# Kernel tuning notes

Measured on AMD Instinct MI355X. Metric: run time of the kernel, lower is better.

Reference implementation:

```python
import jax, jax.numpy as jnp
import numpy as np

B, S, HID, NH = 2, 2048, 2048, 16
HD = HID // NH          # head_size = 128
ROPE_THETA = 10000.0
SCALING = HD ** -0.5


def setup_inputs() -> dict:
    key = jax.random.key(0)
    ks = jax.random.split(key, 8)
    std = 1.0 / np.sqrt(HID)
    inp = {
        "hidden_states": jax.random.normal(ks[0], (B, S, HID), jnp.float32),
        "positions": jnp.broadcast_to(jnp.arange(S, dtype=jnp.int32), (B, S)),
        "wq": jax.random.normal(ks[1], (HID, HID), jnp.float32) * std,
        "bq": jax.random.normal(ks[2], (HID,), jnp.float32) * 0.02,
        "wk": jax.random.normal(ks[3], (HID, HID), jnp.float32) * std,
        "bk": jax.random.normal(ks[4], (HID,), jnp.float32) * 0.02,
        "wv": jax.random.normal(ks[5], (HID, HID), jnp.float32) * std,
        "bv": jax.random.normal(ks[6], (HID,), jnp.float32) * 0.02,
        "wc": jax.random.normal(ks[7], (HID, HID), jnp.float32) * std,
    }
    return inp


def _rope_neox(x, positions):
    # x: [B, S, NH, HD]; positions: [B, S] int
    half = HD // 2
    inv_freq = 1.0 / (ROPE_THETA ** (jnp.arange(half, dtype=jnp.float32) * (2.0 / HD)))
    freqs = positions.astype(jnp.float32)[..., None] * inv_freq      # [B,S,half]
    cos = jnp.cos(freqs)[:, :, None, :]                               # [B,S,1,half]
    sin = jnp.sin(freqs)[:, :, None, :]
    x1, x2 = x[..., :half], x[..., half:]
    return jnp.concatenate([x1 * cos - x2 * sin, x2 * cos + x1 * sin], axis=-1)


def reference(hidden_states, positions, wq, bq, wk, bk, wv, bv, wc):
    # fused QKV projections
    q = hidden_states @ wq + bq
    k = hidden_states @ wk + bk
    v = hidden_states @ wv + bv
    q = q.reshape(B, S, NH, HD)
    k = k.reshape(B, S, NH, HD)
    v = v.reshape(B, S, NH, HD)
    # neox-style rotary embedding over full head dim
    q = _rope_neox(q, positions)
    k = _rope_neox(k, positions)
    # causal self-attention (prefill path of RadixAttention)
    scores = jnp.einsum("bqhd,bkhd->bhqk", q, k) * SCALING
    causal = jnp.tril(jnp.ones((S, S), dtype=bool))
    scores = jnp.where(causal, scores, jnp.finfo(scores.dtype).min)
    probs = jax.nn.softmax(scores, axis=-1)
    attn = jnp.einsum("bhqk,bkhd->bqhd", probs, v).reshape(B, S, HID)
    # output projection (no bias)
    return attn @ wc
```

## Files before the change

kernel.cpp:

```cpp
#include <hip/hip_runtime.h>
#include <stdint.h>

constexpr int Bsz = 2;
constexpr int Ssz = 2048;
constexpr int Hid = 2048;
constexpr int NHd = 16;
constexpr int Hd  = 128;
constexpr int Mrows = Bsz * Ssz;

typedef __bf16 bf16;
typedef __bf16 bf16x8 __attribute__((ext_vector_type(8)));
typedef __bf16 bf16x4 __attribute__((ext_vector_type(4)));
typedef float  f32x4  __attribute__((ext_vector_type(4)));
typedef float  f32x16 __attribute__((ext_vector_type(16)));

__device__ __forceinline__ void gload_lds16(const bf16* g, bf16* l) {
  __builtin_amdgcn_global_load_lds((const __attribute__((address_space(1))) void*)g,
                                   (__attribute__((address_space(3))) void*)l, 16, 0, 0);
}

__device__ __forceinline__ uint32_t pkbf(bf16 a, bf16 b) {
  union { bf16 hh[2]; uint32_t u; } x;
  x.hh[0] = a; x.hh[1] = b;
  return x.u;
}
__device__ __forceinline__ uint32_t pkff(float a, float b) {
  return pkbf((bf16)a, (bf16)b);
}

__global__ void k_cvt(const float* __restrict__ in, bf16* __restrict__ out, int n4) {
  int i = blockIdx.x * blockDim.x + threadIdx.x;
  if (i >= n4) return;
  float4 v = ((const float4*)in)[i];
  bf16x4 o = { (bf16)v.x, (bf16)v.y, (bf16)v.z, (bf16)v.w };
  ((bf16x4*)out)[i] = o;
}

__global__ void k_wtrans(const float* __restrict__ w0, const float* __restrict__ w1,
                         const float* __restrict__ w2, const float* __restrict__ w3,
                         bf16* __restrict__ out) {
  __shared__ float tile[32][33];
  int z = blockIdx.z;
  const float* w = (z == 0) ? w0 : (z == 1) ? w1 : (z == 2) ? w2 : w3;
  bf16* o = out + (size_t)z * Hid * Hid;
  int n0 = blockIdx.x * 32, k0 = blockIdx.y * 32;
  int tx = threadIdx.x, ty = threadIdx.y;
#pragma unroll
  for (int i = 0; i < 4; i++)
    tile[ty + i * 8][tx] = w[(size_t)(k0 + ty + i * 8) * Hid + n0 + tx];
  __syncthreads();
#pragma unroll
  for (int i = 0; i < 4; i++)
    o[(size_t)(n0 + ty + i * 8) * Hid + k0 + tx] = (bf16)tile[tx][ty + i * 8];
}

__device__ __forceinline__ bf16x8 rdfrag(const bf16* t, int row, int kslot) {
  return *(const bf16x8*)((const char*)t + row * 128 + (((kslot ^ (row & 7)) & 7) << 4));
}

template <int NB>
__device__ __forceinline__ void stageN(const bf16* g, bf16* l, int w, int lane) {
  const int rsub = lane >> 3;
  const int slot = (lane & 7) ^ rsub;
#pragma unroll
  for (int j = 0; j < NB; ++j) {
    const int blk = w * NB + j;
    gload_lds16(g + (size_t)(blk * 8 + rsub) * Hid + slot * 8, l + blk * 512);
  }
}

#define PH_SYNC()                                      \
  __builtin_amdgcn_s_barrier();                        \
  asm volatile("s_waitcnt lgkmcnt(0)" ::: "memory");   \
  __builtin_amdgcn_sched_barrier(0);

template <int MODE, int CHM, int CHN>
__global__ __launch_bounds__(512, 1) void k_gemm(const bf16* __restrict__ A,
                                                 const bf16* __restrict__ Bt,
                                                 const float* __restrict__ biasq,
                                                 const float* __restrict__ biask,
                                                 const float* __restrict__ biasv,
                                                 bf16* __restrict__ Qo, bf16* __restrict__ Ko,
                                                 bf16* __restrict__ Vo, float* __restrict__ Fo) {
  constexpr int KK = Hid;
  constexpr int NT = KK / 64;
  __shared__ bf16 smA[3][256 * 64];
  __shared__ bf16 smB[3][128 * 64];
  const int hw = blockIdx.y * gridDim.x + blockIdx.x;
  const int chunk = hw & 7, within = hw >> 3;
  const int chunk_rows = gridDim.y / CHM;
  const int cr = chunk % chunk_rows, cc = chunk / chunk_rows;
  const int mt = cr * CHM + within % CHM;
  const int nt = cc * CHN + within / CHM;
  const int m0 = mt * 256, n0 = nt * 128;
  const int tid = threadIdx.x, lane = tid & 63, w = tid >> 6;
  const int wm = w >> 1, wn = w & 1;
  const int frow = lane & 15, a4 = lane >> 4;
  const bf16* Ag = A + (size_t)m0 * KK;
  const bf16* Bg = Bt + (size_t)n0 * KK;
  f32x4 acc[4][4] = {};
  stageN<4>(Ag, smA[0], w, lane);
  stageN<2>(Bg, smB[0], w, lane);
  stageN<4>(Ag + 64, smA[1], w, lane);
  stageN<2>(Bg + 64, smB[1], w, lane);
  asm volatile("s_waitcnt vmcnt(6)" ::: "memory");
  __builtin_amdgcn_s_barrier();
  for (int kt = 0; kt < NT; ++kt) {
    const bf16* At  = smA[kt % 3];
    const bf16* Btl = smB[kt % 3];
    bf16* As2 = smA[(kt + 2) % 3];
    bf16* Bs2 = smB[(kt + 2) % 3];
    const int kn2 = (kt + 2 < NT ? kt + 2 : kt) * 64;
    bf16x8 af[2][2], bfr[4][2];
#pragma unroll
    for (int mi = 0; mi < 2; ++mi)
#pragma unroll
      for (int kk = 0; kk < 2; ++kk)
        af[mi][kk] = rdfrag(At, wm * 64 + mi * 16 + frow, kk * 4 + a4);
#pragma unroll
    for (int ni = 0; ni < 4; ++ni)
#pragma unroll
      for (int kk = 0; kk < 2; ++kk)
        bfr[ni][kk] = rdfrag(Btl, wn * 64 + ni * 16 + frow, kk * 4 + a4);
    stageN<4>(Ag + kn2, As2, w, lane);
    PH_SYNC();
    __builtin_amdgcn_s_setprio(1);
#pragma unroll
    for (int mi = 0; mi < 2; ++mi)
#pragma unroll
      for (int ni = 0; ni < 4; ++ni)
#pragma unroll
        for (int kk = 0; kk < 2; ++kk)
          acc[mi][ni] = __builtin_amdgcn_mfma_f32_16x16x32_bf16(
              af[mi][kk], bfr[ni][kk], acc[mi][ni], 0, 0, 0);
    __builtin_amdgcn_s_setprio(0);
    __builtin_amdgcn_s_barrier();
#pragma unroll
    for (int mi = 0; mi < 2; ++mi)
#pragma unroll
      for (int kk = 0; kk < 2; ++kk)
        af[mi][kk] = rdfrag(At, wm * 64 + (2 + mi) * 16 + frow, kk * 4 + a4);
    stageN<2>(Bg + kn2, Bs2, w, lane);
    PH_SYNC();
    __builtin_amdgcn_s_setprio(1);
#pragma unroll
    for (int mi = 0; mi < 2; ++mi)
#pragma unroll
      for (int ni = 0; ni < 4; ++ni)
#pragma unroll
        for (int kk = 0; kk < 2; ++kk)
          acc[2 + mi][ni] = __builtin_amdgcn_mfma_f32_16x16x32_bf16(
              af[mi][kk], bfr[ni][kk], acc[2 + mi][ni], 0, 0, 0);
    __builtin_amdgcn_s_setprio(0);
    asm volatile("s_waitcnt vmcnt(6)" ::: "memory");
    __builtin_amdgcn_sched_barrier(0);
    __builtin_amdgcn_s_barrier();
  }
  if (MODE == 0) {
    const int z = n0 >> 11;
    const float* bias = (z == 0) ? biasq : (z == 1) ? biask : biasv;
    bf16* o = (z == 0) ? Qo : (z == 1) ? Ko : Vo;
    const float oscale = (z == 1) ? (float)(0.08838834764831845 * 1.4426950408889634) : 1.0f;
#pragma unroll
    for (int ni = 0; ni < 4; ++ni) {
      const int col = n0 + wn * 64 + ni * 16 + frow;
      const float bb_ = bias[col & 2047];
      const int h = (col >> 7) & 15, hd = col & (Hd - 1);
#pragma unroll
      for (int mi = 0; mi < 4; ++mi) {
#pragma unroll
        for (int r = 0; r < 4; ++r) {
          const int row = m0 + wm * 64 + mi * 16 + a4 * 4 + r;
          const int bb = row >> 11, ss = row & (Ssz - 1);
          o[(((size_t)bb * NHd + h) * Ssz + ss) * Hd + hd] = (bf16)((acc[mi][ni][r] + bb_) * oscale);
        }
      }
    }
  } else {
#pragma unroll
    for (int mi = 0; mi < 4; ++mi)
#pragma unroll
      for (int ni = 0; ni < 4; ++ni) {
        const int col = n0 + wn * 64 + ni * 16 + frow;
#pragma unroll
        for (int r = 0; r < 4; ++r) {
          const int row = m0 + wm * 64 + mi * 16 + a4 * 4 + r;
          Fo[(size_t)row * Hid + col] = acc[mi][ni][r];
        }
      }
  }
}

__global__ void k_rope(bf16* __restrict__ Q, bf16* __restrict__ Kk, const int* __restrict__ pos) {
  const int idx = blockIdx.x * 256 + threadIdx.x;
  const int i = idx & 63;
  const int s = (idx >> 6) & (Ssz - 1);
  const int bh = idx >> 17;
  const int b = bh >> 4;
  const float p = (float)pos[b * Ssz + s];
  const float f = p * exp2f(-(float)i * 0.20762050593046014f);
  float sn, cs;
  sincosf(f, &sn, &cs);
  const size_t base = ((size_t)bh * Ssz + s) * Hd;
  float x1 = (float)Q[base + i], x2 = (float)Q[base + i + 64];
  Q[base + i]      = (bf16)(x1 * cs - x2 * sn);
  Q[base + i + 64] = (bf16)(x2 * cs + x1 * sn);
  x1 = (float)Kk[base + i]; x2 = (float)Kk[base + i + 64];
  Kk[base + i]      = (bf16)(x1 * cs - x2 * sn);
  Kk[base + i + 64] = (bf16)(x2 * cs + x1 * sn);
}

__global__ __launch_bounds__(256, 2) void k_attn(const bf16* __restrict__ Qg,
                                                 const bf16* __restrict__ Kg,
                                                 const bf16* __restrict__ Vg,
                                                 bf16* __restrict__ AO) {
  const int bh = blockIdx.y;
  int qc = blockIdx.x;
  if (bh & 1) qc = 15 - qc;
  const int tid = threadIdx.x, lane = tid & 63, w = tid >> 6;
  const int l31 = lane & 31, h = lane >> 5;
  __shared__ bf16 Ks[2][64 * 128];
  __shared__ bf16 Vt[2][128 * 72];
  const size_t hbase = (size_t)bh * Ssz * Hd;
  const int q0 = qc * 128 + w * 32;
  bf16x8 qf[8];
  {
    const bf16* qp = Qg + hbase + (size_t)(q0 + l31) * Hd + h * 8;
#pragma unroll
    for (int c = 0; c < 8; c++) qf[c] = *(const bf16x8*)(qp + c * 16);
  }
  float m = -1e30f, lsum = 0.f;
  f32x16 o[4] = {};
  const int NT = 2 * (qc + 1);
  const int r4  = (tid >> 4) << 2;
  const int hd0 = (tid & 15) << 3;
  bf16x8 vv[4];
#pragma unroll
  for (int p = 0; p < 4; p++)
    vv[p] = *(const bf16x8*)(Vg + hbase + (size_t)(r4 + p) * Hd + hd0);
  __builtin_amdgcn_sched_barrier(0);
#pragma unroll
  for (int i = 0; i < 4; i++) {
    const int db  = (w * 4 + i) * 1024 + (lane << 4);
    const int row = db >> 8;
    const int cb  = (db & 255) ^ ((row & 7) << 4);
    gload_lds16(Kg + hbase + row * Hd + (cb >> 1), Ks[0] + (w * 4 + i) * 512);
  }
  for (int t = 0; t < NT; ++t) {
    const int kv0 = t * 64;
    const int cur = t & 1;
    asm volatile("s_waitcnt vmcnt(4)" ::: "memory");
#pragma unroll
    for (int j = 0; j < 8; j++) {
      uint2 wv;
      wv.x = pkbf(vv[0][j], vv[1][j]);
      wv.y = pkbf(vv[2][j], vv[3][j]);
      const int hd = hd0 + j;
      const int cb = (r4 * 2) ^ (((hd >> 3) & 7) << 4);
      *(uint2*)((char*)(Vt[cur]) + hd * 144 + cb) = wv;
    }
    const int tn = (t + 1 < NT) ? t + 1 : t;
    const size_t nb = (size_t)tn * 64;
#pragma unroll
    for (int p = 0; p < 4; p++)
      vv[p] = *(const bf16x8*)(Vg + hbase + (nb + r4 + p) * Hd + hd0);
    __builtin_amdgcn_sched_barrier(0);
#pragma unroll
    for (int i = 0; i < 4; i++) {
      const int db  = (w * 4 + i) * 1024 + (lane << 4);
      const int row = db >> 8;
      const int cb  = (db & 255) ^ ((row & 7) << 4);
      gload_lds16(Kg + hbase + (nb + row) * Hd + (cb >> 1), Ks[cur ^ 1] + (w * 4 + i) * 512);
    }
    asm volatile("s_waitcnt vmcnt(8) lgkmcnt(0)" ::: "memory");
    __builtin_amdgcn_sched_barrier(0);
    __builtin_amdgcn_s_barrier();
    if (kv0 <= q0 + 31) {
      const bf16* KsC = Ks[cur];
      const bf16* VtC = Vt[cur];
      f32x16 s0 = {}, s1 = {};
#pragma unroll
      for (int c = 0; c < 8; c++) {
        const int cb = (c * 32 + h * 16) ^ ((l31 & 7) << 4);
        bf16x8 k0 = *(const bf16x8*)((const char*)KsC + l31 * 256 + cb);
        bf16x8 k1 = *(const bf16x8*)((const char*)KsC + (32 + l31) * 256 + cb);
        s0 = __builtin_amdgcn_mfma_f32_32x32x16_bf16(k0, qf[c], s0, 0, 0, 0);
        s1 = __builtin_amdgcn_mfma_f32_32x32x16_bf16(k1, qf[c], s1, 0, 0, 0);
      }
      if (kv0 + 63 > q0) {
        const int qg = q0 + l31;
        const int kb = kv0 + 4 * h;
#pragma unroll
        for (int r = 0; r < 16; r++) {
          const int cr = (r & 3) + 8 * (r >> 2);
          if (kb + cr > qg)      s0[r] = -1e30f;
          if (kb + 32 + cr > qg) s1[r] = -1e30f;
        }
      }
      float tm = s0[0];
#pragma unroll
      for (int r = 1; r < 16; r++) tm = fmaxf(tm, s0[r]);
#pragma unroll
      for (int r = 0; r < 16; r++) tm = fmaxf(tm, s1[r]);
      tm = fmaxf(tm, __shfl_xor(tm, 32));
      if (!__all(tm - m <= 8.0f)) {
        const float mn = fmaxf(m, tm);
        const float rs = exp2f(m - mn);
        m = mn; lsum *= rs;
#pragma unroll
        for (int ct = 0; ct < 4; ct++)
#pragma unroll
          for (int r = 0; r < 16; r++) o[ct][r] *= rs;
      }
      float ps = 0.f;
#pragma unroll
      for (int r = 0; r < 16; r++) { s0[r] = exp2f(s0[r] - m); ps += s0[r]; }
#pragma unroll
      for (int r = 0; r < 16; r++) { s1[r] = exp2f(s1[r] - m); ps += s1[r]; }
      ps += __shfl_xor(ps, 32);
      lsum += ps;
      uint32_t gw[8][2];
#pragma unroll
      for (int g = 0; g < 4; g++) {
        gw[g][0]     = pkff(s0[4 * g], s0[4 * g + 1]);
        gw[g][1]     = pkff(s0[4 * g + 2], s0[4 * g + 3]);
        gw[4 + g][0] = pkff(s1[4 * g], s1[4 * g + 1]);
        gw[4 + g][1] = pkff(s1[4 * g + 2], s1[4 * g + 3]);
      }
#pragma unroll
      for (int kc = 0; kc < 4; kc++) {
        const uint32_t a0 = gw[2 * kc][0], a1 = gw[2 * kc][1];
        const uint32_t b0 = gw[2 * kc + 1][0], b1 = gw[2 * kc + 1][1];
        const uint32_t sd0 = h ? a0 : b0, sd1 = h ? a1 : b1;
        const uint32_t r0 = (uint32_t)__shfl_xor((int)sd0, 32);
        const uint32_t r1 = (uint32_t)__shfl_xor((int)sd1, 32);
        union { uint32_t u[4]; bf16x8 v; } pa;
        pa.u[0] = h ? r0 : a0; pa.u[1] = h ? r1 : a1;
        pa.u[2] = h ? b0 : r0; pa.u[3] = h ? b1 : r1;
#pragma unroll
        for (int ct = 0; ct < 4; ct++) {
          const int row = ct * 32 + l31;
          const int cb = (kc * 32 + h * 16) ^ (((row >> 3) & 7) << 4);
          bf16x8 vf = *(const bf16x8*)((const char*)VtC + row * 144 + cb);
          o[ct] = __builtin_amdgcn_mfma_f32_32x32x16_bf16(pa.v, vf, o[ct], 0, 0, 0);
        }
      }
    }
    __builtin_amdgcn_s_barrier();
  }
  const float linv = 1.0f / lsum;
  float li[16];
#pragma unroll
  for (int r = 0; r < 16; r++)
    li[r] = __shfl(linv, (r & 3) + 8 * (r >> 2) + 4 * h);
  const int b = bh >> 4, hh = bh & 15;
#pragma unroll
  for (int ct = 0; ct < 4; ct++) {
#pragma unroll
    for (int r = 0; r < 16; r++) {
      const int qrow = q0 + (r & 3) + 8 * (r >> 2) + 4 * h;
      AO[((size_t)b * Ssz + qrow) * Hid + hh * Hd + ct * 32 + l31] = (bf16)(o[ct][r] * li[r]);
    }
  }
}

extern "C" void kernel_launch(void* const* d_in, const int* in_sizes, int n_in,
                              void* d_out, int out_size, void* d_ws, size_t ws_size,
                              hipStream_t stream) {
  (void)in_sizes; (void)n_in; (void)out_size; (void)ws_size;
  const float* hidden   = (const float*)d_in[0];
  const int*   positions= (const int*)d_in[1];
  const float* wq = (const float*)d_in[2];
  const float* bq = (const float*)d_in[3];
  const float* wk = (const float*)d_in[4];
  const float* bk = (const float*)d_in[5];
  const float* wv = (const float*)d_in[6];
  const float* bv = (const float*)d_in[7];
  const float* wc = (const float*)d_in[8];
  float* out = (float*)d_out;

  char* ws = (char*)d_ws;
  bf16* WT  = (bf16*)ws;
  bf16* Hbf = (bf16*)(ws + (size_t)4 * Hid * Hid * 2);
  bf16* Qb  = (bf16*)(ws + (size_t)4 * Hid * Hid * 2 + (size_t)Mrows * Hid * 2);
  bf16* Kb  = Qb + (size_t)Mrows * Hid;
  bf16* Vb  = Kb + (size_t)Mrows * Hid;

  k_cvt<<<dim3(Mrows * Hid / 4 / 256), dim3(256), 0, stream>>>(hidden, Hbf, Mrows * Hid / 4);
  k_wtrans<<<dim3(Hid / 32, Hid / 32, 4), dim3(32, 8), 0, stream>>>(wq, wk, wv, wc, WT);
  k_gemm<0, 8, 12><<<dim3(48, 16), dim3(512), 0, stream>>>(
      Hbf, WT, bq, bk, bv, Qb, Kb, Vb, nullptr);
  k_rope<<<dim3(Bsz * NHd * Ssz * 64 / 256), dim3(256), 0, stream>>>(Qb, Kb, positions);
  k_attn<<<dim3(16, Bsz * NHd), dim3(256), 0, stream>>>(Qb, Kb, Vb, Hbf );
  k_gemm<1, 4, 8><<<dim3(16, 16), dim3(512), 0, stream>>>(
      Hbf, WT + (size_t)3 * Hid * Hid, nullptr, nullptr, nullptr,
      nullptr, nullptr, nullptr, out);
}
```

Before: 293.5 us.

## Enlarge GEMM tiles to 256x256 with double-buffered LDS and four-phase loop

Both GEMM launches now use 256x256 output tiles in place of 256x128. The LDS buffering drops from triple to double buffering, and each K step is split into four MFMA phases that overlap the next A and B loads. The goal is more data reuse per LDS byte and fewer reloads from global memory. In exchange each wave holds twice the accumulators, the waitcnt before each barrier is now a full vmcnt(0) that exposes load latency, and the grids shrink to 384 and 128 blocks, which may leave CUs idle on a 256-CU part.

```diff
diff --git a/kernel.cpp b/kernel.cpp
--- a/kernel.cpp
+++ b/kernel.cpp
@@ -75,7 +75,7 @@
   __builtin_amdgcn_sched_barrier(0);
 
 template <int MODE, int CHM, int CHN>
-__global__ __launch_bounds__(512, 1) void k_gemm(const bf16* __restrict__ A,
+__global__ __launch_bounds__(512, 2) void k_gemm(const bf16* __restrict__ A,
                                                  const bf16* __restrict__ Bt,
                                                  const float* __restrict__ biasq,
                                                  const float* __restrict__ biask,
@@ -84,77 +84,64 @@
                                                  bf16* __restrict__ Vo, float* __restrict__ Fo) {
   constexpr int KK = Hid;
   constexpr int NT = KK / 64;
-  __shared__ bf16 smA[3][256 * 64];
-  __shared__ bf16 smB[3][128 * 64];
+  __shared__ bf16 smA[2][256 * 64];
+  __shared__ bf16 smB[2][256 * 64];
   const int hw = blockIdx.y * gridDim.x + blockIdx.x;
   const int chunk = hw & 7, within = hw >> 3;
   const int chunk_rows = gridDim.y / CHM;
   const int cr = chunk % chunk_rows, cc = chunk / chunk_rows;
   const int mt = cr * CHM + within % CHM;
   const int nt = cc * CHN + within / CHM;
-  const int m0 = mt * 256, n0 = nt * 128;
+  const int m0 = mt * 256, n0 = nt * 256;
   const int tid = threadIdx.x, lane = tid & 63, w = tid >> 6;
-  const int wm = w >> 1, wn = w & 1;
+  const int wm = w >> 2, wn = w & 3;
   const int frow = lane & 15, a4 = lane >> 4;
   const bf16* Ag = A + (size_t)m0 * KK;
   const bf16* Bg = Bt + (size_t)n0 * KK;
-  f32x4 acc[4][4] = {};
+  f32x4 acc[8][4] = {};
   stageN<4>(Ag, smA[0], w, lane);
-  stageN<2>(Bg, smB[0], w, lane);
-  stageN<4>(Ag + 64, smA[1], w, lane);
-  stageN<2>(Bg + 64, smB[1], w, lane);
-  asm volatile("s_waitcnt vmcnt(6)" ::: "memory");
+  stageN<4>(Bg, smB[0], w, lane);
+  asm volatile("s_waitcnt vmcnt(0)" ::: "memory");
   __builtin_amdgcn_s_barrier();
   for (int kt = 0; kt < NT; ++kt) {
-    const bf16* At  = smA[kt % 3];
-    const bf16* Btl = smB[kt % 3];
-    bf16* As2 = smA[(kt + 2) % 3];
-    bf16* Bs2 = smB[(kt + 2) % 3];
-    const int kn2 = (kt + 2 < NT ? kt + 2 : kt) * 64;
-    bf16x8 af[2][2], bfr[4][2];
-#pragma unroll
-    for (int mi = 0; mi < 2; ++mi)
+    const bf16* At  = smA[kt & 1];
+    const bf16* Btl = smB[kt & 1];
+    bf16* As2 = smA[(kt + 1) & 1];
+    bf16* Bs2 = smB[(kt + 1) & 1];
+    const int kn = (kt + 1 < NT ? kt + 1 : kt) * 64;
+    bf16x8 bfr[4][2];
+#pragma unroll
+    for (int nf = 0; nf < 4; ++nf)
 #pragma unroll
       for (int kk = 0; kk < 2; ++kk)
-        af[mi][kk] = rdfrag(At, wm * 64 + mi * 16 + frow, kk * 4 + a4);
-#pragma unroll
-    for (int ni = 0; ni < 4; ++ni)
-#pragma unroll
-      for (int kk = 0; kk < 2; ++kk)
-        bfr[ni][kk] = rdfrag(Btl, wn * 64 + ni * 16 + frow, kk * 4 + a4);
-    stageN<4>(Ag + kn2, As2, w, lane);
-    PH_SYNC();
-    __builtin_amdgcn_s_setprio(1);
-#pragma unroll
-    for (int mi = 0; mi < 2; ++mi)
-#pragma unroll
-      for (int ni = 0; ni < 4; ++ni)
+        bfr[nf][kk] = rdfrag(Btl, wn * 64 + nf * 16 + frow, kk * 4 + a4);
+#pragma unroll
+    for (int ph = 0; ph < 4; ++ph) {
+      bf16x8 af[2][2];
+#pragma unroll
+      for (int i = 0; i < 2; ++i)
 #pragma unroll
         for (int kk = 0; kk < 2; ++kk)
-          acc[mi][ni] = __builtin_amdgcn_mfma_f32_16x16x32_bf16(
-              af[mi][kk], bfr[ni][kk], acc[mi][ni], 0, 0, 0);
-    __builtin_amdgcn_s_setprio(0);
-    __builtin_amdgcn_s_barrier();
-#pragma unroll
-    for (int mi = 0; mi < 2; ++mi)
-#pragma unroll
-      for (int kk = 0; kk < 2; ++kk)
-        af[mi][kk] = rdfrag(At, wm * 64 + (2 + mi) * 16 + frow, kk * 4 + a4);
-    stageN<2>(Bg + kn2, Bs2, w, lane);
-    PH_SYNC();
-    __builtin_amdgcn_s_setprio(1);
-#pragma unroll
-    for (int mi = 0; mi < 2; ++mi)
-#pragma unroll
-      for (int ni = 0; ni < 4; ++ni)
-#pragma unroll
-        for (int kk = 0; kk < 2; ++kk)
-          acc[2 + mi][ni] = __builtin_amdgcn_mfma_f32_16x16x32_bf16(
-              af[mi][kk], bfr[ni][kk], acc[2 + mi][ni], 0, 0, 0);
-    __builtin_amdgcn_s_setprio(0);
-    asm volatile("s_waitcnt vmcnt(6)" ::: "memory");
-    __builtin_amdgcn_sched_barrier(0);
-    __builtin_amdgcn_s_barrier();
+          af[i][kk] = rdfrag(At, wm * 128 + (ph * 2 + i) * 16 + frow, kk * 4 + a4);
+      if (ph == 0) stageN<4>(Ag + kn, As2, w, lane);
+      if (ph == 1) stageN<4>(Bg + kn, Bs2, w, lane);
+      PH_SYNC();
+      __builtin_amdgcn_s_setprio(1);
+#pragma unroll
+      for (int i = 0; i < 2; ++i)
+#pragma unroll
+        for (int nf = 0; nf < 4; ++nf)
+#pragma unroll
+          for (int kk = 0; kk < 2; ++kk)
+            acc[ph * 2 + i][nf] = __builtin_amdgcn_mfma_f32_16x16x32_bf16(
+                af[i][kk], bfr[nf][kk], acc[ph * 2 + i][nf], 0, 0, 0);
+      __builtin_amdgcn_s_setprio(0);
+      if (ph == 3) {
+        asm volatile("s_waitcnt vmcnt(0)" ::: "memory");
+        __builtin_amdgcn_sched_barrier(0);
+      }
+      __builtin_amdgcn_s_barrier();
+    }
   }
   if (MODE == 0) {
     const int z = n0 >> 11;
@@ -162,30 +149,30 @@
     bf16* o = (z == 0) ? Qo : (z == 1) ? Ko : Vo;
     const float oscale = (z == 1) ? (float)(0.08838834764831845 * 1.4426950408889634) : 1.0f;
 #pragma unroll
-    for (int ni = 0; ni < 4; ++ni) {
-      const int col = n0 + wn * 64 + ni * 16 + frow;
+    for (int nf = 0; nf < 4; ++nf) {
+      const int col = n0 + wn * 64 + nf * 16 + frow;
       const float bb_ = bias[col & 2047];
       const int h = (col >> 7) & 15, hd = col & (Hd - 1);
 #pragma unroll
-      for (int mi = 0; mi < 4; ++mi) {
+      for (int mf = 0; mf < 8; ++mf) {
 #pragma unroll
         for (int r = 0; r < 4; ++r) {
-          const int row = m0 + wm * 64 + mi * 16 + a4 * 4 + r;
+          const int row = m0 + wm * 128 + mf * 16 + a4 * 4 + r;
           const int bb = row >> 11, ss = row & (Ssz - 1);
-          o[(((size_t)bb * NHd + h) * Ssz + ss) * Hd + hd] = (bf16)((acc[mi][ni][r] + bb_) * oscale);
+          o[(((size_t)bb * NHd + h) * Ssz + ss) * Hd + hd] = (bf16)((acc[mf][nf][r] + bb_) * oscale);
         }
       }
     }
   } else {
 #pragma unroll
-    for (int mi = 0; mi < 4; ++mi)
-#pragma unroll
-      for (int ni = 0; ni < 4; ++ni) {
-        const int col = n0 + wn * 64 + ni * 16 + frow;
+    for (int mf = 0; mf < 8; ++mf)
+#pragma unroll
+      for (int nf = 0; nf < 4; ++nf) {
+        const int col = n0 + wn * 64 + nf * 16 + frow;
 #pragma unroll
         for (int r = 0; r < 4; ++r) {
-          const int row = m0 + wm * 64 + mi * 16 + a4 * 4 + r;
-          Fo[(size_t)row * Hid + col] = acc[mi][ni][r];
+          const int row = m0 + wm * 128 + mf * 16 + a4 * 4 + r;
+          Fo[(size_t)row * Hid + col] = acc[mf][nf][r];
         }
       }
   }
@@ -388,11 +375,11 @@
 
   k_cvt<<<dim3(Mrows * Hid / 4 / 256), dim3(256), 0, stream>>>(hidden, Hbf, Mrows * Hid / 4);
   k_wtrans<<<dim3(Hid / 32, Hid / 32, 4), dim3(32, 8), 0, stream>>>(wq, wk, wv, wc, WT);
-  k_gemm<0, 8, 12><<<dim3(48, 16), dim3(512), 0, stream>>>(
+  k_gemm<0, 8, 6><<<dim3(24, 16), dim3(512), 0, stream>>>(
       Hbf, WT, bq, bk, bv, Qb, Kb, Vb, nullptr);
   k_rope<<<dim3(Bsz * NHd * Ssz * 64 / 256), dim3(256), 0, stream>>>(Qb, Kb, positions);
   k_attn<<<dim3(16, Bsz * NHd), dim3(256), 0, stream>>>(Qb, Kb, Vb, Hbf );
-  k_gemm<1, 4, 8><<<dim3(16, 16), dim3(512), 0, stream>>>(
+  k_gemm<1, 8, 2><<<dim3(8, 16), dim3(512), 0, stream>>>(
       Hbf, WT + (size_t)3 * Hid * Hid, nullptr, nullptr, nullptr,
       nullptr, nullptr, nullptr, out);
 }
```

Result: slower. 331.2 us (+12.9%).
